# Performance work log

Hardware: AMD Instinct MI355X
Metric: run time of the kernel (lower is better)

Reference implementation:

```python
import jax, jax.numpy as jnp
import numpy as np

H = 768; R = 16; L = 3; NS = 128; NQ = 128


def setup_inputs():
    key = jax.random.key(0)
    ks = iter(jax.random.split(key, 40))
    def w(shape, s=0.02):
        return (s * jax.random.normal(next(ks), shape)).astype(jnp.float32)
    return {
        "support_features": jax.random.normal(next(ks), (NS, H), jnp.float32),
        "support_labels": jax.random.randint(next(ks), (NS,), 0, 3),
        "query_features": jax.random.normal(next(ks), (NQ, H), jnp.float32),
        "sim_w1": w((H, 2 * H)), "sim_b1": jnp.zeros((H,), jnp.float32),
        "sim_w2": w((R, H)), "sim_b2": jnp.zeros((R,), jnp.float32),
        "div_w1": w((H, 2 * H)), "div_b1": jnp.zeros((H,), jnp.float32),
        "div_w2": w((R, H)), "div_b2": jnp.zeros((R,), jnp.float32),
        "rel_w": w((L, R, H, H)), "rel_b": jnp.zeros((L, R, H), jnp.float32),
        "agg_w1": w((L, H, 2 * H)), "agg_b1": jnp.zeros((L, H), jnp.float32),
        "agg_w2": w((L, H, H)), "agg_b2": jnp.zeros((L, H), jnp.float32),
        "ln_g": jnp.ones((L, H), jnp.float32), "ln_b": jnp.zeros((L, H), jnp.float32),
        "cls_w1": w((H // 2, H)), "cls_b1": jnp.zeros((H // 2,), jnp.float32),
        "cls_w2": w((3, H // 2)), "cls_b2": jnp.zeros((3,), jnp.float32),
    }


def _symmetrize(F):
    # torch loop fills [i,j] and [j,i] with value computed from pair (min(i,j), max(i,j)); diag stays 0
    N = F.shape[0]
    idx = jnp.arange(N)
    lower = (idx[:, None] > idx[None, :])
    Fs = jnp.where(lower[:, :, None], jnp.swapaxes(F, 0, 1), F)
    off = (idx[:, None] != idx[None, :]).astype(F.dtype)
    return Fs * off[:, :, None]


def _relations(x, w1, b1, w2, b2, diversity):
    h = x.shape[1]
    wa, wb = w1[:, :h], w1[:, h:]  # split concat([a,b]) @ w1^T into two matmuls
    pa = x @ wa.T                  # [N,H], contribution of first element (x_i)
    if diversity:
        d = jnp.abs(x[:, None, :] - x[None, :, :])   # [N,N,H]
        hid = jax.nn.relu(pa[:, None, :] + d @ wb.T + b1)
    else:
        pb = x @ wb.T
        hid = jax.nn.relu(pa[:, None, :] + pb[None, :, :] + b1)
    logits = hid @ w2.T + b2       # [N,N,R]
    return _symmetrize(jax.nn.softmax(logits, axis=-1))


def _layer_norm(y, g, b):
    mu = y.mean(-1, keepdims=True)
    var = ((y - mu) ** 2).mean(-1, keepdims=True)
    return (y - mu) / jnp.sqrt(var + 1e-5) * g + b


def _prop_layer(x, C, rw, rb, aw1, ab1, aw2, ab2, g, b):
    N = x.shape[0]
    T = jnp.einsum('jh,rkh->jrk', x, rw) + rb       # per-relation transform [N,R,H]
    msg = jnp.einsum('ijr,jrk->ik', C, T) / (N - 1)  # mean over N-1 neighbors (diag of C is 0)
    comb = jnp.concatenate([x, msg], axis=-1)
    agg = jax.nn.relu(comb @ aw1.T + ab1) @ aw2.T + ab2
    return _layer_norm(agg + x, g, b)


def reference(support_features, support_labels, query_features,
              sim_w1, sim_b1, sim_w2, sim_b2,
              div_w1, div_b1, div_w2, div_b2,
              rel_w, rel_b, agg_w1, agg_b1, agg_w2, agg_b2, ln_g, ln_b,
              cls_w1, cls_b1, cls_w2, cls_b2):
    all_x = jnp.concatenate([support_features, query_features], axis=0)
    sim = _relations(all_x, sim_w1, sim_b1, sim_w2, sim_b2, diversity=False)
    div = _relations(all_x, div_w1, div_b1, div_w2, div_b2, diversity=True)
    C = (sim + div) * 0.5
    x = all_x
    for l in range(L):
        x = _prop_layer(x, C, rel_w[l], rel_b[l], agg_w1[l], agg_b1[l],
                        agg_w2[l], agg_b2[l], ln_g[l], ln_b[l])
    q = x[support_features.shape[0]:]
    preds = jax.nn.relu(q @ cls_w1.T + cls_b1) @ cls_w2.T + cls_b2  # dropout = identity (eval)
    return preds, sim, div, x
```

## Files before the change

kernel.cpp:

```cpp
#include <hip/hip_runtime.h>
#include <hip/hip_bf16.h>
#include <hip/hip_fp16.h>


typedef __attribute__((ext_vector_type(8))) short s16x8;
typedef __attribute__((ext_vector_type(4))) float f32x4;

__device__ __forceinline__ short f2bf_s(float f){
  union { __hip_bfloat16 h; short s; } u; u.h = __float2bfloat16(f); return u.s;
}
__device__ __forceinline__ float bf_s2f(short s){
  union { __hip_bfloat16 h; short s; } u; u.s = s; return __bfloat162float(u.h);
}
__device__ __forceinline__ short f2h_s(float f){
  union { __half h; short s; } u; u.h = __float2half(f); return u.s;
}
__device__ __forceinline__ f32x4 mfma16(s16x8 a, s16x8 b, f32x4 c){
  return __builtin_amdgcn_mfma_f32_16x16x32_bf16(a, b, c, 0, 0, 0);
}
__device__ __forceinline__ f32x4 mfma16h(s16x8 a, s16x8 b, f32x4 c){
  return __builtin_amdgcn_mfma_f32_16x16x32_f16(a, b, c, 0, 0, 0);
}
__device__ __forceinline__ void gload16(void* lds, const void* g){
  __builtin_amdgcn_global_load_lds((const __attribute__((address_space(1))) void*)g,
                                   (__attribute__((address_space(3))) void*)lds,
                                   16, 0, 0);
}
__device__ __forceinline__ unsigned pack2bf(float lo, float hi){
  return __builtin_amdgcn_perm(__float_as_uint(hi), __float_as_uint(lo), 0x07060302u);
}
__device__ __forceinline__ s16x8 absdiff_h(uint4 a, uint4 b){
  union { s16x8 v; unsigned u[4]; } o;
  const unsigned au[4] = {a.x,a.y,a.z,a.w}, bu[4] = {b.x,b.y,b.z,b.w};
  #pragma unroll
  for (int w = 0; w < 4; ++w){
    unsigned d;
    asm("v_pk_add_f16 %0, %1, %2 neg_lo:[0,1] neg_hi:[0,1]"
        : "=v"(d) : "v"(au[w]), "v"(bu[w]));
    o.u[w] = d & 0x7fff7fffu;
  }
  return o.v;
}

__device__ __forceinline__ void tri_decode(int b, int& i0, int& j0){
  int jb = (int)((sqrtf(2.f*(float)b + 1.f) - 1.f)*0.5f);
  while (2*(jb+1)*(jb+2) <= b) ++jb;
  while (2*jb*(jb+1) > b) --jb;
  i0 = (b - 2*jb*(jb+1))*4;
  j0 = jb*16;
}
__device__ __forceinline__ void tri_decode8x32(int b, int& i0, int& j0){
  int jb = (int)((sqrtf(2.f*(float)b + 1.f) - 1.f)*0.5f);
  while (2*(jb+1)*(jb+2) <= b) ++jb;
  while (2*jb*(jb+1) > b) --jb;
  i0 = (b - 2*jb*(jb+1))*8;
  j0 = jb*32;
}

template<int BM, int BN, int EPI>
__global__ __launch_bounds__(256) void gemm_bt2(
    const short* __restrict__ A, int lda,
    const short* __restrict__ B, int ldb,
    float* __restrict__ Cf, short* __restrict__ Cb, int ldc,
    const float* __restrict__ bias, int K, int NT)
{
  __shared__ short As[BM*128];
  __shared__ short Bs[BN*128];
  const int tid = threadIdx.x, lane = tid & 63, wid = tid >> 6;
  const int nt = blockIdx.x % NT, mt = blockIdx.x / NT;
  const int m0 = mt*BM, n0 = nt*BN;
  const int wm0 = (wid>>1)*(BM/2), wn0 = (wid&1)*(BN/2);
  f32x4 acc[BM/32][BN/32] = {};
  for (int k0 = 0; k0 < K; k0 += 128){
    if (k0) __syncthreads();
    #pragma unroll
    for (int q = 0; q < BM/16; ++q){
      const int d = (wid*(BM/16)+q)*1024 + lane*16;
      const int row = d>>8, c = d&255;
      gload16((char*)As + (wid*(BM/16)+q)*1024,
              (const char*)A + (size_t)(m0+row)*lda*2 + (size_t)k0*2 + (c ^ ((row&7)<<4)));
    }
    #pragma unroll
    for (int q = 0; q < BN/16; ++q){
      const int d = (wid*(BN/16)+q)*1024 + lane*16;
      const int row = d>>8, c = d&255;
      gload16((char*)Bs + (wid*(BN/16)+q)*1024,
              (const char*)B + (size_t)(n0+row)*ldb*2 + (size_t)k0*2 + (c ^ ((row&7)<<4)));
    }
    __syncthreads();
    #pragma unroll
    for (int kk = 0; kk < 4; ++kk){
      const int colb = (kk*32 + (lane>>4)*8)*2;
      s16x8 af[BM/32], bfv[BN/32];
      #pragma unroll
      for (int mi = 0; mi < BM/32; ++mi){
        const int row = wm0 + mi*16 + (lane&15);
        af[mi] = *(const s16x8*)((char*)As + row*256 + (colb ^ ((row&7)<<4)));
      }
      #pragma unroll
      for (int ni = 0; ni < BN/32; ++ni){
        const int row = wn0 + ni*16 + (lane&15);
        bfv[ni] = *(const s16x8*)((char*)Bs + row*256 + (colb ^ ((row&7)<<4)));
      }
      #pragma unroll
      for (int mi = 0; mi < BM/32; ++mi)
        #pragma unroll
        for (int ni = 0; ni < BN/32; ++ni)
          acc[mi][ni] = mfma16(af[mi], bfv[ni], acc[mi][ni]);
    }
  }
  #pragma unroll
  for (int mi = 0; mi < BM/32; ++mi){
    #pragma unroll
    for (int ni = 0; ni < BN/32; ++ni){
      const int gcol = n0 + wn0 + ni*16 + (lane&15);
      const float bv = bias[gcol];
      #pragma unroll
      for (int r = 0; r < 4; ++r){
        const int grow = m0 + wm0 + mi*16 + (lane>>4)*4 + r;
        float v = acc[mi][ni][r] + bv;
        if (EPI == 2) v = fmaxf(v, 0.f);
        if (EPI == 3) Cf[(size_t)grow*ldc + gcol] = v;
        else          Cb[(size_t)grow*ldc + gcol] = f2bf_s(v);
      }
    }
  }
}

__global__ __launch_bounds__(256) void gemm_msg(
    const short* __restrict__ A,
    const short* __restrict__ B,
    float* __restrict__ slabs)
{
  __shared__ short As[64*64];
  __shared__ short Bs[64*64];
  const int tid = threadIdx.x, lane = tid & 63, wid = tid >> 6;
  const int mt = blockIdx.x / 12, nt = blockIdx.x % 12;
  const int m0 = mt*64, n0 = nt*64, kc0 = blockIdx.y*512;
  const int wm0 = (wid>>1)*32, wn0 = (wid&1)*32;
  f32x4 acc[2][2] = {};
  for (int s = 0; s < 8; ++s){
    const int k0 = kc0 + s*64;
    if (s) __syncthreads();
    #pragma unroll
    for (int q = 0; q < 2; ++q){
      const int d = (wid*2+q)*1024 + lane*16;
      const int row = d>>7, c = d&127;
      gload16((char*)As + (wid*2+q)*1024,
              (const char*)A + (size_t)(m0+row)*8192 + (size_t)k0*2 + (c ^ ((row&7)<<4)));
    }
    #pragma unroll
    for (int rd = 0; rd < 2; ++rd){
      int ei = rd*2048 + tid*8, kr = ei>>6, nc = ei&63;
      union { uint4 v; short s4[8]; } u;
      u.v = *(const uint4*)(B + (size_t)(k0+kr)*768 + n0 + nc);
      #pragma unroll
      for (int e = 0; e < 8; ++e)
        *(short*)((char*)Bs + (nc+e)*128 + ((kr*2) ^ (((nc+e)&7)<<4))) = u.s4[e];
    }
    __syncthreads();
    #pragma unroll
    for (int kk = 0; kk < 2; ++kk){
      const int colb = (kk*32 + (lane>>4)*8)*2;
      s16x8 af[2], bfv[2];
      #pragma unroll
      for (int mi = 0; mi < 2; ++mi){
        const int row = wm0 + mi*16 + (lane&15);
        af[mi] = *(const s16x8*)((char*)As + row*128 + (colb ^ ((row&7)<<4)));
      }
      #pragma unroll
      for (int ni = 0; ni < 2; ++ni){
        const int row = wn0 + ni*16 + (lane&15);
        bfv[ni] = *(const s16x8*)((char*)Bs + row*128 + (colb ^ ((row&7)<<4)));
      }
      #pragma unroll
      for (int mi = 0; mi < 2; ++mi)
        #pragma unroll
        for (int ni = 0; ni < 2; ++ni)
          acc[mi][ni] = mfma16(af[mi], bfv[ni], acc[mi][ni]);
    }
  }
  float* out = slabs + (size_t)blockIdx.y*196608;
  #pragma unroll
  for (int mi = 0; mi < 2; ++mi)
    #pragma unroll
    for (int ni = 0; ni < 2; ++ni){
      const int gcol = n0 + wn0 + ni*16 + (lane&15);
      #pragma unroll
      for (int r = 0; r < 4; ++r){
        const int grow = m0 + wm0 + mi*16 + (lane>>4)*4 + r;
        out[(size_t)grow*768 + gcol] = acc[mi][ni][r];
      }
    }
}

__global__ void msgsum(const float* __restrict__ slabs, short* __restrict__ comb){
  const int i = (blockIdx.x*256 + threadIdx.x)*4;
  if (i >= 196608) return;
  float4 s = {0.f,0.f,0.f,0.f};
  #pragma unroll
  for (int c = 0; c < 8; ++c){
    float4 v = *(const float4*)(slabs + (size_t)c*196608 + i);
    s.x += v.x; s.y += v.y; s.z += v.z; s.w += v.w;
  }
  const float sc = 1.f/255.f;
  const int row = i/768, col = i%768;
  union { uint2 u; short s4[4]; } o;
  o.s4[0]=f2bf_s(s.x*sc); o.s4[1]=f2bf_s(s.y*sc);
  o.s4[2]=f2bf_s(s.z*sc); o.s4[3]=f2bf_s(s.w*sc);
  *(uint2*)(comb + (size_t)row*1536 + 768 + col) = o.u;
}

__global__ __launch_bounds__(512, 2) void pairrel7(
    const short* __restrict__ xh,
    const short* __restrict__ wbdh,
    const float* __restrict__ P2,
    const short* __restrict__ w2d_g,
    float* __restrict__ Ldp)
{
  __shared__ short Bs[2*256*64];
  const int tid = threadIdx.x, lane = tid & 63, wv = tid >> 6;
  const int ip = wv >> 2, jj = (wv >> 1) & 1, wc = wv & 1;
  int i0, j0; tri_decode8x32(blockIdx.x, i0, j0);
  const int nt = blockIdx.y, n0 = nt*256;

  const short* xjp = xh + (size_t)(j0 + jj*16 + (lane&15))*768 + (lane>>4)*8;
  const short* xib = xh + (size_t)(i0 + 4*ip)*768 + (lane>>4)*8;

  #pragma unroll
  for (int q = 0; q < 4; ++q){
    const int d = (wv*4+q)*1024 + lane*16;
    const int row = d>>7, c = d&127;
    gload16((char*)Bs + (wv*4+q)*1024,
            (const char*)wbdh + (size_t)(n0+row)*1536 + (c ^ ((row&7)<<4)));
  }

  f32x4 acc[4][8] = {};
  for (int t = 0; t < 12; ++t){
    uint4 uja = *(const uint4*)(xjp + t*64);
    uint4 ujb = *(const uint4*)(xjp + t*64 + 32);
    uint4 uia[4], uib[4];
    #pragma unroll
    for (int mi = 0; mi < 4; ++mi){
      uia[mi] = *(const uint4*)(xib + (size_t)mi*768 + t*64);
      uib[mi] = *(const uint4*)(xib + (size_t)mi*768 + t*64 + 32);
    }
    if (t < 11){
      char* dst = (char*)Bs + ((t+1)&1)*32768;
      const char* src = (const char*)wbdh + (size_t)(t+1)*128;
      #pragma unroll
      for (int q = 0; q < 4; ++q){
        const int d = (wv*4+q)*1024 + lane*16;
        const int row = d>>7, c = d&127;
        gload16(dst + (wv*4+q)*1024, src + (size_t)(n0+row)*1536 + (c ^ ((row&7)<<4)));
      }
    }
    __builtin_amdgcn_sched_barrier(0);
    if (t < 11) asm volatile("s_waitcnt vmcnt(14)" ::: "memory");
    else        asm volatile("s_waitcnt vmcnt(10)" ::: "memory");
    __builtin_amdgcn_s_barrier();
    __builtin_amdgcn_sched_barrier(0);
    const char* bufc = (const char*)Bs + (t&1)*32768;
    #pragma unroll
    for (int kk = 0; kk < 2; ++kk){
      s16x8 af[4];
      #pragma unroll
      for (int mi = 0; mi < 4; ++mi)
        af[mi] = absdiff_h(kk ? ujb : uja, kk ? uib[mi] : uia[mi]);
      const int colb = (kk*32 + (lane>>4)*8)*2;
      #pragma unroll
      for (int ni = 0; ni < 8; ++ni){
        const int row = wc*128 + ni*16 + (lane&15);
        s16x8 bv = *(const s16x8*)(bufc + row*128 + (colb ^ ((row&7)<<4)));
        #pragma unroll
        for (int mi = 0; mi < 4; ++mi)
          acc[mi][ni] = mfma16h(af[mi], bv, acc[mi][ni]);
      }
    }
    __builtin_amdgcn_sched_barrier(0);
    __builtin_amdgcn_s_barrier();
  }
  __syncthreads();

  float* red = (float*)((char*)Bs + 32768);
  const int kh = wv >> 2, rq = wv & 3;
  #pragma unroll
  for (int h = 0; h < 4; ++h){
    if (ip == (h>>1)){
      #pragma unroll
      for (int q = 0; q < 2; ++q){
        const int mi = 2*(h&1) + q;
        const float* pr = P2 + (size_t)(i0 + 4*ip + mi)*2304 + 1536 + n0;
        #pragma unroll
        for (int ni = 0; ni < 8; ++ni){
          const int col = wc*128 + ni*16 + (lane&15);
          const float pav = pr[col];
          #pragma unroll
          for (int r = 0; r < 4; ++r){
            const int lrow = q*32 + jj*16 + (lane>>4)*4 + r;
            const float v = fmaxf(acc[mi][ni][r] + pav, 0.f);
            *(short*)((char*)Bs + lrow*512 + ((col*2) ^ ((lrow&7)<<4))) =
                (short)(__float_as_uint(v) >> 16);
          }
        }
      }
    }
    __syncthreads();
    f32x4 a2 = {0.f,0.f,0.f,0.f};
    const int arow = rq*16 + (lane&15);
    #pragma unroll
    for (int qq = 0; qq < 4; ++qq){
      const int k = kh*128 + qq*32 + (lane>>4)*8;
      s16x8 a = *(const s16x8*)((char*)Bs + arow*512 + ((k*2) ^ ((arow&7)<<4)));
      s16x8 w = *(const s16x8*)(w2d_g + (size_t)(lane&15)*768 + n0 + k);
      a2 = mfma16(a, w, a2);
    }
    if (kh == 1){
      #pragma unroll
      for (int r = 0; r < 4; ++r)
        red[(rq*16 + (lane>>4)*4 + r)*16 + (lane&15)] = a2[r];
    }
    __syncthreads();
    if (kh == 0){
      #pragma unroll
      for (int r = 0; r < 4; ++r){
        const int lrow = rq*16 + (lane>>4)*4 + r;
        const int p = h*64 + lrow;
        const int i = i0 + (p>>5), j = j0 + (p&31);
        Ldp[(size_t)nt*1048576 + (((size_t)i<<8) + j)*16 + (lane&15)]
          = a2[r] + red[lrow*16 + (lane&15)];
      }
    }
    __syncthreads();
  }
}

__global__ __launch_bounds__(256) void simfused(
    const float* __restrict__ P2,
    const short* __restrict__ w2s_g,
    const float* __restrict__ Ldp,
    const float* __restrict__ b2s, const float* __restrict__ b2d,
    float* __restrict__ simo, float* __restrict__ divo, short* __restrict__ CBo)
{
  __shared__ short Hs[64*256];
  const int tid = threadIdx.x, lane = tid & 63, wv = tid >> 6;
  int i0, j0; tri_decode(blockIdx.x, i0, j0);
  const int arow = wv*16 + (lane&15);
  f32x4 acc2 = {0.f,0.f,0.f,0.f};
  for (int nt = 0; nt < 3; ++nt){
    const int n0 = nt*256;
    if (nt) __syncthreads();
    {
      const int row = tid>>2, c0 = (tid&3)*64;
      const float* pap = P2 + (size_t)(i0 + (row>>4))*2304 + n0 + c0;
      const float* pbp = P2 + (size_t)(j0 + (row&15))*2304 + 768 + n0 + c0;
      #pragma unroll
      for (int cc = 0; cc < 64; cc += 8){
        float4 a0 = *(const float4*)(pap+cc), a1 = *(const float4*)(pap+cc+4);
        float4 q0 = *(const float4*)(pbp+cc), q1 = *(const float4*)(pbp+cc+4);
        uint4 o;
        o.x = pack2bf(fmaxf(a0.x+q0.x,0.f), fmaxf(a0.y+q0.y,0.f));
        o.y = pack2bf(fmaxf(a0.z+q0.z,0.f), fmaxf(a0.w+q0.w,0.f));
        o.z = pack2bf(fmaxf(a1.x+q1.x,0.f), fmaxf(a1.y+q1.y,0.f));
        o.w = pack2bf(fmaxf(a1.z+q1.z,0.f), fmaxf(a1.w+q1.w,0.f));
        *(uint4*)((char*)Hs + row*512 + (((c0+cc)*2) ^ ((row&7)<<4))) = o;
      }
    }
    __syncthreads();
    #pragma unroll
    for (int q = 0; q < 8; ++q){
      const int colb = (q*32 + (lane>>4)*8)*2;
      s16x8 a = *(const s16x8*)((const char*)Hs + arow*512 + (colb ^ ((arow&7)<<4)));
      s16x8 w = *(const s16x8*)(w2s_g + (size_t)(lane&15)*768 + n0 + q*32 + (lane>>4)*8);
      acc2 = mfma16(a, w, acc2);
    }
  }
  const int r_ = lane & 15;
  const float bs_ = b2s[r_], bd_ = b2d[r_];
  #pragma unroll
  for (int r = 0; r < 4; ++r){
    const int p = wv*16 + (lane>>4)*4 + r;
    const int i = i0 + (p>>4), j = j0 + (p&15);
    if (j < i) continue;
    if (j == i){
      const size_t pii = (((size_t)i<<8) + i)*16 + r_;
      simo[pii] = 0.f; divo[pii] = 0.f; CBo[pii] = 0;
      continue;
    }
    const size_t base = (((size_t)i<<8) + j)*16;
    const float sv = acc2[r] + bs_;
    const float dv = Ldp[base+r_] + Ldp[base+1048576+r_] + Ldp[base+2097152+r_] + bd_;
    float m = sv;
    m = fmaxf(m, __shfl_xor(m,1)); m = fmaxf(m, __shfl_xor(m,2));
    m = fmaxf(m, __shfl_xor(m,4)); m = fmaxf(m, __shfl_xor(m,8));
    float e = expf(sv - m), s = e;
    s += __shfl_xor(s,1); s += __shfl_xor(s,2); s += __shfl_xor(s,4); s += __shfl_xor(s,8);
    const float so = e/s;
    m = dv;
    m = fmaxf(m, __shfl_xor(m,1)); m = fmaxf(m, __shfl_xor(m,2));
    m = fmaxf(m, __shfl_xor(m,4)); m = fmaxf(m, __shfl_xor(m,8));
    e = expf(dv - m); s = e;
    s += __shfl_xor(s,1); s += __shfl_xor(s,2); s += __shfl_xor(s,4); s += __shfl_xor(s,8);
    const float dd = e/s;
    const size_t pij = base + r_;
    const size_t pji = (((size_t)j<<8) + i)*16 + r_;
    simo[pij] = so; simo[pji] = so;
    divo[pij] = dd; divo[pji] = dd;
    const short cb = f2bf_s(0.5f*(so + dd));
    CBo[pij] = cb; CBo[pji] = cb;
  }
}

__global__ __launch_bounds__(512) void gemm_relT(
    const short* __restrict__ A,
    const float* __restrict__ Bf,
    short* __restrict__ T,
    const float* __restrict__ bias)
{
  __shared__ short As[256*64];
  __shared__ short Bs[64*64];
  const int tid = threadIdx.x, lane = tid & 63, wv = tid >> 6;
  const int n0 = blockIdx.x*64;
  const int wm = wv >> 1, wn = wv & 1;
  const int brow = tid >> 3, c0 = (tid & 7)*8;
  f32x4 acc[4][2] = {};
  for (int k0 = 0; k0 < 768; k0 += 64){
    if (k0) __syncthreads();
    #pragma unroll
    for (int q = 0; q < 4; ++q){
      const int d = (wv*4+q)*1024 + lane*16;
      const int row = d>>7, c = d&127;
      gload16((char*)As + (wv*4+q)*1024,
              (const char*)A + (size_t)row*3072 + (size_t)k0*2 + (c ^ ((row&7)<<4)));
    }
    {
      const float* bp = Bf + (size_t)(n0+brow)*768 + k0 + c0;
      float4 v0 = *(const float4*)bp, v1 = *(const float4*)(bp+4);
      union { uint4 v; unsigned u[4]; } uo;
      uo.u[0]=pack2bf(v0.x,v0.y); uo.u[1]=pack2bf(v0.z,v0.w);
      uo.u[2]=pack2bf(v1.x,v1.y); uo.u[3]=pack2bf(v1.z,v1.w);
      *(uint4*)((char*)Bs + brow*128 + (((c0*2)) ^ ((brow&7)<<4))) = uo.v;
    }
    __syncthreads();
    #pragma unroll
    for (int kk = 0; kk < 2; ++kk){
      const int kb = kk*64 + (lane>>4)*16;
      s16x8 af[4], bfv[2];
      #pragma unroll
      for (int mi = 0; mi < 4; ++mi){
        const int row = wm*64 + mi*16 + (lane&15);
        af[mi] = *(const s16x8*)((char*)As + row*128 + (kb ^ ((row&7)<<4)));
      }
      #pragma unroll
      for (int ni = 0; ni < 2; ++ni){
        const int row = wn*32 + ni*16 + (lane&15);
        bfv[ni] = *(const s16x8*)((char*)Bs + row*128 + (kb ^ ((row&7)<<4)));
      }
      #pragma unroll
      for (int mi = 0; mi < 4; ++mi)
        #pragma unroll
        for (int ni = 0; ni < 2; ++ni)
          acc[mi][ni] = mfma16(af[mi], bfv[ni], acc[mi][ni]);
    }
  }
  #pragma unroll
  for (int mi = 0; mi < 4; ++mi)
    #pragma unroll
    for (int ni = 0; ni < 2; ++ni){
      const int nn = n0 + wn*32 + ni*16 + (lane&15);
      const float bv = bias[nn];
      #pragma unroll
      for (int r = 0; r < 4; ++r){
        const int row = wm*64 + mi*16 + (lane>>4)*4 + r;
        T[(size_t)row*12288 + nn] = f2bf_s(acc[mi][ni][r] + bv);
      }
    }
}

__global__ __launch_bounds__(256) void ln_kernel(
    const float* __restrict__ y, float* __restrict__ x, short* __restrict__ combx,
    const float* __restrict__ g, const float* __restrict__ b, float* __restrict__ xfinal)
{
  const int row = blockIdx.x, tid = threadIdx.x;
  float tv[3]; float s = 0.f, s2 = 0.f;
  #pragma unroll
  for (int c = 0; c < 3; ++c){
    const int idx = tid + c*256;
    const float v = y[row*768+idx] + x[row*768+idx];
    tv[c] = v; s += v; s2 += v*v;
  }
  #pragma unroll
  for (int off = 32; off > 0; off >>= 1){ s += __shfl_down(s, off); s2 += __shfl_down(s2, off); }
  __shared__ float red[8];
  const int wid = tid >> 6, lane = tid & 63;
  if (lane == 0){ red[wid] = s; red[wid+4] = s2; }
  __syncthreads();
  if (tid == 0){
    red[0] = red[0]+red[1]+red[2]+red[3];
    red[4] = red[4]+red[5]+red[6]+red[7];
  }
  __syncthreads();
  const float mu = red[0]*(1.f/768.f);
  const float var = red[4]*(1.f/768.f) - mu*mu;
  const float inv = rsqrtf(var + 1e-5f);
  #pragma unroll
  for (int c = 0; c < 3; ++c){
    const int idx = tid + c*256;
    const float v = (tv[c]-mu)*inv*g[idx] + b[idx];
    x[row*768+idx] = v;
    combx[(size_t)row*1536 + idx] = f2bf_s(v);
    if (xfinal) xfinal[row*768+idx] = v;
  }
}

__device__ __forceinline__ void cvt4(const float* __restrict__ s,
                                     short* __restrict__ d, int i, int n){
  if (i >= n) return;
  float4 v = *(const float4*)(s+i);
  union { uint2 u; short s4[4]; } o;
  o.s4[0]=f2bf_s(v.x); o.s4[1]=f2bf_s(v.y); o.s4[2]=f2bf_s(v.z); o.s4[3]=f2bf_s(v.w);
  *(uint2*)(d+i) = o.u;
}

__global__ void setup_all(
    const float* __restrict__ sim_w2, const float* __restrict__ div_w2,
    const float* __restrict__ agg_w1, const float* __restrict__ agg_w2,
    const float* __restrict__ cls_w1, const float* __restrict__ sim_w1,
    const float* __restrict__ div_w1, const float* __restrict__ sup,
    const float* __restrict__ qry, const float* __restrict__ sim_b1,
    const float* __restrict__ div_b1,
    short* __restrict__ W2S, short* __restrict__ W2D, short* __restrict__ AW1,
    short* __restrict__ AW2, short* __restrict__ CW1, short* __restrict__ W1X4,
    float* __restrict__ XF, short* __restrict__ COMB, float* __restrict__ B1C,
    short* __restrict__ XH, short* __restrict__ WBDH)
{
  const int b = blockIdx.x, tid = threadIdx.x;
  if (b < 12)        cvt4(sim_w2, W2S, (b*256+tid)*4, 12288);
  else if (b < 24)   cvt4(div_w2, W2D, ((b-12)*256+tid)*4, 12288);
  else if (b < 3480) cvt4(agg_w1, AW1, ((b-24)*256+tid)*4, 3538944);
  else if (b < 5208) cvt4(agg_w2, AW2, ((b-3480)*256+tid)*4, 1769472);
  else if (b < 5496) cvt4(cls_w1, CW1, ((b-5208)*256+tid)*4, 294912);
  else if (b < 7800){
    const int i = ((b-5496)*256+tid)*4;
    if (i < 2359296){
      const int mat = i / 589824, rem = i % 589824;
      const int r = rem / 768, c = rem % 768;
      const float* src = (mat < 2 ? sim_w1 : div_w1) + (size_t)r*1536 + (mat&1)*768 + c;
      float4 v = *(const float4*)src;
      union { uint2 u; short s4[4]; } o;
      o.s4[0]=f2bf_s(v.x); o.s4[1]=f2bf_s(v.y); o.s4[2]=f2bf_s(v.z); o.s4[3]=f2bf_s(v.w);
      *(uint2*)(W1X4+i) = o.u;
    }
  } else if (b < 7992){
    const int i = ((b-7800)*256+tid)*4;
    if (i < 196608){
      const int row = i / 768, col = i % 768;
      const float* s = (row < 128 ? sup + (size_t)row*768 : qry + (size_t)(row-128)*768) + col;
      float4 v = *(const float4*)s;
      *(float4*)(XF+i) = v;
      union { uint2 u; short s4[4]; } o;
      o.s4[0]=f2bf_s(v.x); o.s4[1]=f2bf_s(v.y); o.s4[2]=f2bf_s(v.z); o.s4[3]=f2bf_s(v.w);
      *(uint2*)(COMB + (size_t)row*1536 + col) = o.u;
      union { uint2 u; short s4[4]; } oh;
      oh.s4[0]=f2h_s(v.x); oh.s4[1]=f2h_s(v.y); oh.s4[2]=f2h_s(v.z); oh.s4[3]=f2h_s(v.w);
      *(uint2*)(XH + i) = oh.u;
    }
  } else if (b < 7993){
    for (int t = tid; t < 2304; t += 256)
      B1C[t] = (t < 768) ? sim_b1[t] : ((t < 1536) ? 0.f : div_b1[t-1536]);
  } else {
    const int i = ((b-7993)*256+tid)*4;
    if (i < 589824){
      const int r = i / 768, c = i % 768;
      float4 v = *(const float4*)(div_w1 + (size_t)r*1536 + 768 + c);
      union { uint2 u; short s4[4]; } o;
      o.s4[0]=f2h_s(v.x); o.s4[1]=f2h_s(v.y); o.s4[2]=f2h_s(v.z); o.s4[3]=f2h_s(v.w);
      *(uint2*)(WBDH + i) = o.u;
    }
  }
}

__global__ void cls2_kernel(const short* __restrict__ hc, const float* __restrict__ w2,
                            const float* __restrict__ b2, float* __restrict__ preds){
  const int t = blockIdx.x*192 + threadIdx.x;
  if (t >= 384) return;
  const int m = t/3, c = t - m*3;
  float s = b2[c];
  for (int k = 0; k < 384; ++k)
    s += bf_s2f(hc[m*384+k]) * w2[c*384+k];
  preds[m*3+c] = s;
}

static const size_t OFF_B1CAT = 0;
static const size_t OFF_MSGF  = 4210688;
static const size_t OFF_LDP   = 10502144;
static const size_t OFF_P     = 23085056;
static const size_t OFF_XF    = 25444352;
static const size_t OFF_Y     = 26230784;
static const size_t OFF_COMB  = 27017216;
static const size_t OFF_CB    = 27803648;
static const size_t OFF_W1X4  = 29900800;
static const size_t OFF_W2S   = 34619392;
static const size_t OFF_W2D   = 34643968;
static const size_t OFF_AW1   = 34668544;
static const size_t OFF_AW2   = 41746432;
static const size_t OFF_CW1   = 45285376;
static const size_t OFF_TBUF  = 45875200;
static const size_t OFF_HID1  = 52166656;
static const size_t OFF_HIDC  = 52559872;
static const size_t OFF_XH    = 52658176;
static const size_t OFF_WBDH  = 53051392;

extern "C" void kernel_launch(void* const* d_in, const int* in_sizes, int n_in,
                              void* d_out, int out_size, void* d_ws, size_t ws_size,
                              hipStream_t stream)
{
  (void)in_sizes; (void)n_in; (void)out_size; (void)ws_size;
  const float* sup    = (const float*)d_in[0];
  const float* qry    = (const float*)d_in[2];
  const float* sim_w1 = (const float*)d_in[3];
  const float* sim_b1 = (const float*)d_in[4];
  const float* sim_w2 = (const float*)d_in[5];
  const float* sim_b2 = (const float*)d_in[6];
  const float* div_w1 = (const float*)d_in[7];
  const float* div_b1 = (const float*)d_in[8];
  const float* div_w2 = (const float*)d_in[9];
  const float* div_b2 = (const float*)d_in[10];
  const float* rel_w  = (const float*)d_in[11];
  const float* rel_b  = (const float*)d_in[12];
  const float* agg_w1 = (const float*)d_in[13];
  const float* agg_b1 = (const float*)d_in[14];
  const float* agg_w2 = (const float*)d_in[15];
  const float* agg_b2 = (const float*)d_in[16];
  const float* ln_g   = (const float*)d_in[17];
  const float* ln_b   = (const float*)d_in[18];
  const float* cls_w1 = (const float*)d_in[19];
  const float* cls_b1 = (const float*)d_in[20];
  const float* cls_w2 = (const float*)d_in[21];
  const float* cls_b2 = (const float*)d_in[22];

  char* w = (char*)d_ws;
  float* B1C  = (float*)(w + OFF_B1CAT);
  float* MSGF = (float*)(w + OFF_MSGF);
  float* LDP  = (float*)(w + OFF_LDP);
  float* P2   = (float*)(w + OFF_P);
  float* XF   = (float*)(w + OFF_XF);
  float* Y    = (float*)(w + OFF_Y);
  short* COMB = (short*)(w + OFF_COMB);
  short* CB   = (short*)(w + OFF_CB);
  short* W1X4 = (short*)(w + OFF_W1X4);
  short* W2S  = (short*)(w + OFF_W2S);
  short* W2D  = (short*)(w + OFF_W2D);
  short* AW1  = (short*)(w + OFF_AW1);
  short* AW2  = (short*)(w + OFF_AW2);
  short* CW1  = (short*)(w + OFF_CW1);
  short* TBUF = (short*)(w + OFF_TBUF);
  short* HID1 = (short*)(w + OFF_HID1);
  short* HIDC = (short*)(w + OFF_HIDC);
  short* XH   = (short*)(w + OFF_XH);
  short* WBDH = (short*)(w + OFF_WBDH);

  float* preds = (float*)d_out;
  float* simo  = preds + 384;
  float* divo  = simo + 1048576;
  float* xout  = divo + 1048576;

  setup_all<<<8569, 256, 0, stream>>>(sim_w2, div_w2, agg_w1, agg_w2, cls_w1,
                                      sim_w1, div_w1, sup, qry, sim_b1, div_b1,
                                      W2S, W2D, AW1, AW2, CW1, W1X4, XF, COMB, B1C,
                                      XH, WBDH);

  gemm_bt2<32,64,3><<<288, 256, 0, stream>>>(COMB, 1536, W1X4, 768, P2, nullptr, 2304,
                                             B1C, 768, 36);

  pairrel7<<<dim3(144,3), 512, 0, stream>>>(XH, WBDH, P2, W2D, LDP);
  simfused<<<544, 256, 0, stream>>>(P2, W2S, LDP, sim_b2, div_b2, simo, divo, CB);

  for (int l = 0; l < 3; ++l){
    gemm_relT<<<192, 512, 0, stream>>>(COMB, rel_w + (size_t)l*9437184, TBUF,
                                       rel_b + l*12288);
    gemm_msg<<<dim3(48,8), 256, 0, stream>>>(CB, TBUF, MSGF);
    msgsum<<<192, 256, 0, stream>>>(MSGF, COMB);
    gemm_bt2<32,32,2><<<192, 256, 0, stream>>>(COMB, 1536, AW1 + (size_t)l*1179648, 1536,
                                               nullptr, HID1, 768, agg_b1 + l*768, 1536, 24);
    gemm_bt2<32,32,3><<<192, 256, 0, stream>>>(HID1, 768, AW2 + (size_t)l*589824, 768,
                                               Y, nullptr, 768, agg_b2 + l*768, 768, 24);
    ln_kernel<<<256, 256, 0, stream>>>(Y, XF, COMB, ln_g + l*768, ln_b + l*768,
                                       (l == 2) ? xout : nullptr);
  }

  gemm_bt2<32,32,2><<<48, 256, 0, stream>>>(COMB + (size_t)128*1536, 1536, CW1, 768,
                                            nullptr, HIDC, 384, cls_b1, 768, 12);
  cls2_kernel<<<2, 192, 0, stream>>>(HIDC, cls_w2, cls_b2, preds);
}
```

Baseline: 309.7 us.

## Fuse propagation layers and classifier into one cooperative persistent kernel

```diff
diff --git a/kernel.cpp b/kernel.cpp
--- a/kernel.cpp
+++ b/kernel.cpp
@@ -1,6 +1,9 @@
 #include <hip/hip_runtime.h>
 #include <hip/hip_bf16.h>
 #include <hip/hip_fp16.h>
+#include <hip/hip_cooperative_groups.h>
+
+namespace cg = cooperative_groups;
 
 
 typedef __attribute__((ext_vector_type(8))) short s16x8;
@@ -127,16 +130,153 @@
   }
 }
 
-__global__ __launch_bounds__(256) void gemm_msg(
-    const short* __restrict__ A,
-    const short* __restrict__ B,
-    float* __restrict__ slabs)
-{
-  __shared__ short As[64*64];
-  __shared__ short Bs[64*64];
+template<int BM, int BN, int EPI>
+__device__ __forceinline__ void gemm_dev(char* smem_, int b,
+    const short* A, int lda, const short* B, int ldb,
+    float* Cf, short* Cb, int ldc, const float* bias, int K, int NT)
+{
+  short* As = (short*)smem_;
+  short* Bs = (short*)(smem_ + (size_t)BM*256);
   const int tid = threadIdx.x, lane = tid & 63, wid = tid >> 6;
-  const int mt = blockIdx.x / 12, nt = blockIdx.x % 12;
-  const int m0 = mt*64, n0 = nt*64, kc0 = blockIdx.y*512;
+  const int nt = b % NT, mt = b / NT;
+  const int m0 = mt*BM, n0 = nt*BN;
+  const int wm0 = (wid>>1)*(BM/2), wn0 = (wid&1)*(BN/2);
+  f32x4 acc[BM/32][BN/32] = {};
+  for (int k0 = 0; k0 < K; k0 += 128){
+    if (k0) __syncthreads();
+    #pragma unroll
+    for (int q = 0; q < BM/16; ++q){
+      const int d = (wid*(BM/16)+q)*1024 + lane*16;
+      const int row = d>>8, c = d&255;
+      gload16((char*)As + (wid*(BM/16)+q)*1024,
+              (const char*)A + (size_t)(m0+row)*lda*2 + (size_t)k0*2 + (c ^ ((row&7)<<4)));
+    }
+    #pragma unroll
+    for (int q = 0; q < BN/16; ++q){
+      const int d = (wid*(BN/16)+q)*1024 + lane*16;
+      const int row = d>>8, c = d&255;
+      gload16((char*)Bs + (wid*(BN/16)+q)*1024,
+              (const char*)B + (size_t)(n0+row)*ldb*2 + (size_t)k0*2 + (c ^ ((row&7)<<4)));
+    }
+    __syncthreads();
+    #pragma unroll
+    for (int kk = 0; kk < 4; ++kk){
+      const int colb = (kk*32 + (lane>>4)*8)*2;
+      s16x8 af[BM/32], bfv[BN/32];
+      #pragma unroll
+      for (int mi = 0; mi < BM/32; ++mi){
+        const int row = wm0 + mi*16 + (lane&15);
+        af[mi] = *(const s16x8*)((char*)As + row*256 + (colb ^ ((row&7)<<4)));
+      }
+      #pragma unroll
+      for (int ni = 0; ni < BN/32; ++ni){
+        const int row = wn0 + ni*16 + (lane&15);
+        bfv[ni] = *(const s16x8*)((char*)Bs + row*256 + (colb ^ ((row&7)<<4)));
+      }
+      #pragma unroll
+      for (int mi = 0; mi < BM/32; ++mi)
+        #pragma unroll
+        for (int ni = 0; ni < BN/32; ++ni)
+          acc[mi][ni] = mfma16(af[mi], bfv[ni], acc[mi][ni]);
+    }
+  }
+  __syncthreads();
+  #pragma unroll
+  for (int mi = 0; mi < BM/32; ++mi){
+    #pragma unroll
+    for (int ni = 0; ni < BN/32; ++ni){
+      const int gcol = n0 + wn0 + ni*16 + (lane&15);
+      const float bv = bias[gcol];
+      #pragma unroll
+      for (int r = 0; r < 4; ++r){
+        const int grow = m0 + wm0 + mi*16 + (lane>>4)*4 + r;
+        float v = acc[mi][ni][r] + bv;
+        if (EPI == 2) v = fmaxf(v, 0.f);
+        if (EPI == 3) Cf[(size_t)grow*ldc + gcol] = v;
+        else          Cb[(size_t)grow*ldc + gcol] = f2bf_s(v);
+      }
+    }
+  }
+}
+
+__device__ __forceinline__ void relT_dev(char* smem_, int b,
+    const short* A, const float* Bf, short* T, const float* bias)
+{
+  short* As = (short*)smem_;
+  short* Bs = (short*)(smem_ + 16384);
+  const int tid = threadIdx.x, lane = tid & 63, wv = tid >> 6;
+  const int nt = b >> 1, mt = b & 1;
+  const int n0 = nt*64, m0 = mt*128;
+  const int wm = wv >> 1, wn = wv & 1;
+  const int brow = tid >> 2, q4 = tid & 3;
+  f32x4 acc[4][2] = {};
+  for (int k0 = 0; k0 < 768; k0 += 64){
+    if (k0) __syncthreads();
+    #pragma unroll
+    for (int q = 0; q < 4; ++q){
+      const int d = (wv*4+q)*1024 + lane*16;
+      const int row = d>>7, c = d&127;
+      gload16((char*)As + (wv*4+q)*1024,
+              (const char*)A + (size_t)(m0+row)*3072 + (size_t)k0*2 + (c ^ ((row&7)<<4)));
+    }
+    {
+      const float* bp = Bf + (size_t)(n0+brow)*768 + k0 + q4*16;
+      float4 v0 = *(const float4*)bp,      v1 = *(const float4*)(bp+4);
+      float4 v2 = *(const float4*)(bp+8),  v3 = *(const float4*)(bp+12);
+      union { uint4 v; unsigned u[4]; } ua, ub;
+      ua.u[0]=pack2bf(v0.x,v0.y); ua.u[1]=pack2bf(v0.z,v0.w);
+      ua.u[2]=pack2bf(v1.x,v1.y); ua.u[3]=pack2bf(v1.z,v1.w);
+      ub.u[0]=pack2bf(v2.x,v2.y); ub.u[1]=pack2bf(v2.z,v2.w);
+      ub.u[2]=pack2bf(v3.x,v3.y); ub.u[3]=pack2bf(v3.z,v3.w);
+      const int bc = q4*32;
+      *(uint4*)((char*)Bs + brow*128 + ((bc   ) ^ ((brow&7)<<4))) = ua.v;
+      *(uint4*)((char*)Bs + brow*128 + ((bc+16) ^ ((brow&7)<<4))) = ub.v;
+    }
+    __syncthreads();
+    #pragma unroll
+    for (int kk = 0; kk < 2; ++kk){
+      const int kb = kk*64 + (lane>>4)*16;
+      s16x8 af[4], bfv[2];
+      #pragma unroll
+      for (int mi = 0; mi < 4; ++mi){
+        const int row = wm*64 + mi*16 + (lane&15);
+        af[mi] = *(const s16x8*)((char*)As + row*128 + (kb ^ ((row&7)<<4)));
+      }
+      #pragma unroll
+      for (int ni = 0; ni < 2; ++ni){
+        const int row = wn*32 + ni*16 + (lane&15);
+        bfv[ni] = *(const s16x8*)((char*)Bs + row*128 + (kb ^ ((row&7)<<4)));
+      }
+      #pragma unroll
+      for (int mi = 0; mi < 4; ++mi)
+        #pragma unroll
+        for (int ni = 0; ni < 2; ++ni)
+          acc[mi][ni] = mfma16(af[mi], bfv[ni], acc[mi][ni]);
+    }
+  }
+  __syncthreads();
+  #pragma unroll
+  for (int mi = 0; mi < 4; ++mi)
+    #pragma unroll
+    for (int ni = 0; ni < 2; ++ni){
+      const int nn = n0 + wn*32 + ni*16 + (lane&15);
+      const float bv = bias[nn];
+      #pragma unroll
+      for (int r = 0; r < 4; ++r){
+        const int row = m0 + wm*64 + mi*16 + (lane>>4)*4 + r;
+        T[(size_t)row*12288 + nn] = f2bf_s(acc[mi][ni][r] + bv);
+      }
+    }
+}
+
+__device__ __forceinline__ void msg_dev(char* smem_, int t48, int kc,
+    const short* A, const short* B, float* slabs)
+{
+  short* As = (short*)smem_;
+  short* Bs = (short*)(smem_ + 8192);
+  const int tid = threadIdx.x, lane = tid & 63, wid = tid >> 6;
+  const int mt = t48 / 12, nt = t48 % 12;
+  const int m0 = mt*64, n0 = nt*64, kc0 = kc*512;
   const int wm0 = (wid>>1)*32, wn0 = (wid&1)*32;
   f32x4 acc[2][2] = {};
   for (int s = 0; s < 8; ++s){
@@ -180,7 +320,8 @@
           acc[mi][ni] = mfma16(af[mi], bfv[ni], acc[mi][ni]);
     }
   }
-  float* out = slabs + (size_t)blockIdx.y*196608;
+  __syncthreads();
+  float* out = slabs + (size_t)kc*196608;
   #pragma unroll
   for (int mi = 0; mi < 2; ++mi)
     #pragma unroll
@@ -194,21 +335,103 @@
     }
 }
 
-__global__ void msgsum(const float* __restrict__ slabs, short* __restrict__ comb){
-  const int i = (blockIdx.x*256 + threadIdx.x)*4;
-  if (i >= 196608) return;
-  float4 s = {0.f,0.f,0.f,0.f};
-  #pragma unroll
-  for (int c = 0; c < 8; ++c){
-    float4 v = *(const float4*)(slabs + (size_t)c*196608 + i);
-    s.x += v.x; s.y += v.y; s.z += v.z; s.w += v.w;
-  }
-  const float sc = 1.f/255.f;
-  const int row = i/768, col = i%768;
-  union { uint2 u; short s4[4]; } o;
-  o.s4[0]=f2bf_s(s.x*sc); o.s4[1]=f2bf_s(s.y*sc);
-  o.s4[2]=f2bf_s(s.z*sc); o.s4[3]=f2bf_s(s.w*sc);
-  *(uint2*)(comb + (size_t)row*1536 + 768 + col) = o.u;
+__device__ __forceinline__ void ln_dev(char* smem_, int row,
+    const float* y, float* x, short* combx,
+    const float* g, const float* b, float* xfinal)
+{
+  float* red = (float*)smem_;
+  const int tid = threadIdx.x;
+  float tv[3]; float s = 0.f, s2 = 0.f;
+  #pragma unroll
+  for (int c = 0; c < 3; ++c){
+    const int idx = tid + c*256;
+    const float v = y[row*768+idx] + x[row*768+idx];
+    tv[c] = v; s += v; s2 += v*v;
+  }
+  #pragma unroll
+  for (int off = 32; off > 0; off >>= 1){ s += __shfl_down(s, off); s2 += __shfl_down(s2, off); }
+  const int wid = tid >> 6, lane = tid & 63;
+  if (lane == 0){ red[wid] = s; red[wid+4] = s2; }
+  __syncthreads();
+  if (tid == 0){
+    red[0] = red[0]+red[1]+red[2]+red[3];
+    red[4] = red[4]+red[5]+red[6]+red[7];
+  }
+  __syncthreads();
+  const float mu = red[0]*(1.f/768.f);
+  const float var = red[4]*(1.f/768.f) - mu*mu;
+  const float inv = rsqrtf(var + 1e-5f);
+  #pragma unroll
+  for (int c = 0; c < 3; ++c){
+    const int idx = tid + c*256;
+    const float v = (tv[c]-mu)*inv*g[idx] + b[idx];
+    x[row*768+idx] = v;
+    combx[(size_t)row*1536 + idx] = f2bf_s(v);
+    if (xfinal) xfinal[row*768+idx] = v;
+  }
+}
+
+__global__ __launch_bounds__(256) void layers_coop(
+    const float* rel_w, const float* rel_b,
+    short* COMB, const short* CB, short* TBUF, float* MSGF,
+    const short* AW1, const float* agg_b1,
+    const short* AW2, const float* agg_b2,
+    const float* ln_g, const float* ln_b,
+    float* XF, float* Y, short* HID1, float* xout,
+    const short* CW1, const float* cls_b1, short* HIDC,
+    const float* cls_w2, const float* cls_b2, float* preds)
+{
+  cg::grid_group grid = cg::this_grid();
+  __shared__ char smem[24576];
+  const int gb = blockIdx.x, tid = threadIdx.x;
+
+  for (int l = 0; l < 3; ++l){
+    for (int b = gb; b < 384; b += 256)
+      relT_dev(smem, b, COMB, rel_w + (size_t)l*9437184, TBUF, rel_b + l*12288);
+    grid.sync();
+    for (int b = gb; b < 384; b += 256)
+      msg_dev(smem, b % 48, b / 48, CB, TBUF, MSGF);
+    grid.sync();
+    if (gb < 192){
+      const int i = (gb*256 + tid)*4;
+      float4 s = {0.f,0.f,0.f,0.f};
+      #pragma unroll
+      for (int c = 0; c < 8; ++c){
+        float4 v = *(const float4*)(MSGF + (size_t)c*196608 + i);
+        s.x += v.x; s.y += v.y; s.z += v.z; s.w += v.w;
+      }
+      const float sc = 1.f/255.f;
+      const int row = i/768, col = i%768;
+      union { uint2 u; short s4[4]; } o;
+      o.s4[0]=f2bf_s(s.x*sc); o.s4[1]=f2bf_s(s.y*sc);
+      o.s4[2]=f2bf_s(s.z*sc); o.s4[3]=f2bf_s(s.w*sc);
+      *(uint2*)(COMB + (size_t)row*1536 + 768 + col) = o.u;
+    }
+    grid.sync();
+    if (gb < 192)
+      gemm_dev<32,32,2>(smem, gb, COMB, 1536, AW1 + (size_t)l*1179648, 1536,
+                        nullptr, HID1, 768, agg_b1 + l*768, 1536, 24);
+    grid.sync();
+    if (gb < 192)
+      gemm_dev<32,32,3>(smem, gb, HID1, 768, AW2 + (size_t)l*589824, 768,
+                        Y, nullptr, 768, agg_b2 + l*768, 768, 24);
+    grid.sync();
+    ln_dev(smem, gb, Y, XF, COMB, ln_g + l*768, ln_b + l*768,
+           (l == 2) ? xout : nullptr);
+    grid.sync();
+  }
+  if (gb < 48)
+    gemm_dev<32,32,2>(smem, gb, COMB + (size_t)128*1536, 1536, CW1, 768,
+                      nullptr, HIDC, 384, cls_b1, 768, 12);
+  grid.sync();
+  if (gb < 2 && tid < 192){
+    const int t = gb*192 + tid;
+    const int m = t/3, c = t - m*3;
+    float s = cls_b2[c];
+    for (int k = 0; k < 384; ++k)
+      s += bf_s2f(HIDC[m*384+k]) * cls_w2[c*384+k];
+    preds[m*3+c] = s;
+  }
 }
 
 __global__ __launch_bounds__(512, 2) void pairrel7(
@@ -411,108 +634,6 @@
   }
 }
 
-__global__ __launch_bounds__(512) void gemm_relT(
-    const short* __restrict__ A,
-    const float* __restrict__ Bf,
-    short* __restrict__ T,
-    const float* __restrict__ bias)
-{
-  __shared__ short As[256*64];
-  __shared__ short Bs[64*64];
-  const int tid = threadIdx.x, lane = tid & 63, wv = tid >> 6;
-  const int n0 = blockIdx.x*64;
-  const int wm = wv >> 1, wn = wv & 1;
-  const int brow = tid >> 3, c0 = (tid & 7)*8;
-  f32x4 acc[4][2] = {};
-  for (int k0 = 0; k0 < 768; k0 += 64){
-    if (k0) __syncthreads();
-    #pragma unroll
-    for (int q = 0; q < 4; ++q){
-      const int d = (wv*4+q)*1024 + lane*16;
-      const int row = d>>7, c = d&127;
-      gload16((char*)As + (wv*4+q)*1024,
-              (const char*)A + (size_t)row*3072 + (size_t)k0*2 + (c ^ ((row&7)<<4)));
-    }
-    {
-      const float* bp = Bf + (size_t)(n0+brow)*768 + k0 + c0;
-      float4 v0 = *(const float4*)bp, v1 = *(const float4*)(bp+4);
-      union { uint4 v; unsigned u[4]; } uo;
-      uo.u[0]=pack2bf(v0.x,v0.y); uo.u[1]=pack2bf(v0.z,v0.w);
-      uo.u[2]=pack2bf(v1.x,v1.y); uo.u[3]=pack2bf(v1.z,v1.w);
-      *(uint4*)((char*)Bs + brow*128 + (((c0*2)) ^ ((brow&7)<<4))) = uo.v;
-    }
-    __syncthreads();
-    #pragma unroll
-    for (int kk = 0; kk < 2; ++kk){
-      const int kb = kk*64 + (lane>>4)*16;
-      s16x8 af[4], bfv[2];
-      #pragma unroll
-      for (int mi = 0; mi < 4; ++mi){
-        const int row = wm*64 + mi*16 + (lane&15);
-        af[mi] = *(const s16x8*)((char*)As + row*128 + (kb ^ ((row&7)<<4)));
-      }
-      #pragma unroll
-      for (int ni = 0; ni < 2; ++ni){
-        const int row = wn*32 + ni*16 + (lane&15);
-        bfv[ni] = *(const s16x8*)((char*)Bs + row*128 + (kb ^ ((row&7)<<4)));
-      }
-      #pragma unroll
-      for (int mi = 0; mi < 4; ++mi)
-        #pragma unroll
-        for (int ni = 0; ni < 2; ++ni)
-          acc[mi][ni] = mfma16(af[mi], bfv[ni], acc[mi][ni]);
-    }
-  }
-  #pragma unroll
-  for (int mi = 0; mi < 4; ++mi)
-    #pragma unroll
-    for (int ni = 0; ni < 2; ++ni){
-      const int nn = n0 + wn*32 + ni*16 + (lane&15);
-      const float bv = bias[nn];
-      #pragma unroll
-      for (int r = 0; r < 4; ++r){
-        const int row = wm*64 + mi*16 + (lane>>4)*4 + r;
-        T[(size_t)row*12288 + nn] = f2bf_s(acc[mi][ni][r] + bv);
-      }
-    }
-}
-
-__global__ __launch_bounds__(256) void ln_kernel(
-    const float* __restrict__ y, float* __restrict__ x, short* __restrict__ combx,
-    const float* __restrict__ g, const float* __restrict__ b, float* __restrict__ xfinal)
-{
-  const int row = blockIdx.x, tid = threadIdx.x;
-  float tv[3]; float s = 0.f, s2 = 0.f;
-  #pragma unroll
-  for (int c = 0; c < 3; ++c){
-    const int idx = tid + c*256;
-    const float v = y[row*768+idx] + x[row*768+idx];
-    tv[c] = v; s += v; s2 += v*v;
-  }
-  #pragma unroll
-  for (int off = 32; off > 0; off >>= 1){ s += __shfl_down(s, off); s2 += __shfl_down(s2, off); }
-  __shared__ float red[8];
-  const int wid = tid >> 6, lane = tid & 63;
-  if (lane == 0){ red[wid] = s; red[wid+4] = s2; }
-  __syncthreads();
-  if (tid == 0){
-    red[0] = red[0]+red[1]+red[2]+red[3];
-    red[4] = red[4]+red[5]+red[6]+red[7];
-  }
-  __syncthreads();
-  const float mu = red[0]*(1.f/768.f);
-  const float var = red[4]*(1.f/768.f) - mu*mu;
-  const float inv = rsqrtf(var + 1e-5f);
-  #pragma unroll
-  for (int c = 0; c < 3; ++c){
-    const int idx = tid + c*256;
-    const float v = (tv[c]-mu)*inv*g[idx] + b[idx];
-    x[row*768+idx] = v;
-    combx[(size_t)row*1536 + idx] = f2bf_s(v);
-    if (xfinal) xfinal[row*768+idx] = v;
-  }
-}
-
 __device__ __forceinline__ void cvt4(const float* __restrict__ s,
                                      short* __restrict__ d, int i, int n){
   if (i >= n) return;
@@ -578,17 +699,6 @@
       *(uint2*)(WBDH + i) = o.u;
     }
   }
-}
-
-__global__ void cls2_kernel(const short* __restrict__ hc, const float* __restrict__ w2,
-                            const float* __restrict__ b2, float* __restrict__ preds){
-  const int t = blockIdx.x*192 + threadIdx.x;
-  if (t >= 384) return;
-  const int m = t/3, c = t - m*3;
-  float s = b2[c];
-  for (int k = 0; k < 384; ++k)
-    s += bf_s2f(hc[m*384+k]) * w2[c*384+k];
-  preds[m*3+c] = s;
 }
 
 static const size_t OFF_B1CAT = 0;
@@ -676,20 +786,13 @@
   pairrel7<<<dim3(144,3), 512, 0, stream>>>(XH, WBDH, P2, W2D, LDP);
   simfused<<<544, 256, 0, stream>>>(P2, W2S, LDP, sim_b2, div_b2, simo, divo, CB);
 
-  for (int l = 0; l < 3; ++l){
-    gemm_relT<<<192, 512, 0, stream>>>(COMB, rel_w + (size_t)l*9437184, TBUF,
-                                       rel_b + l*12288);
-    gemm_msg<<<dim3(48,8), 256, 0, stream>>>(CB, TBUF, MSGF);
-    msgsum<<<192, 256, 0, stream>>>(MSGF, COMB);
-    gemm_bt2<32,32,2><<<192, 256, 0, stream>>>(COMB, 1536, AW1 + (size_t)l*1179648, 1536,
-                                               nullptr, HID1, 768, agg_b1 + l*768, 1536, 24);
-    gemm_bt2<32,32,3><<<192, 256, 0, stream>>>(HID1, 768, AW2 + (size_t)l*589824, 768,
-                                               Y, nullptr, 768, agg_b2 + l*768, 768, 24);
-    ln_kernel<<<256, 256, 0, stream>>>(Y, XF, COMB, ln_g + l*768, ln_b + l*768,
-                                       (l == 2) ? xout : nullptr);
-  }
-
-  gemm_bt2<32,32,2><<<48, 256, 0, stream>>>(COMB + (size_t)128*1536, 1536, CW1, 768,
-                                            nullptr, HIDC, 384, cls_b1, 768, 12);
-  cls2_kernel<<<2, 192, 0, stream>>>(HIDC, cls_w2, cls_b2, preds);
-}
+  void* cargs[] = {
+    (void*)&rel_w, (void*)&rel_b, (void*)&COMB, (void*)&CB, (void*)&TBUF,
+    (void*)&MSGF, (void*)&AW1, (void*)&agg_b1, (void*)&AW2, (void*)&agg_b2,
+    (void*)&ln_g, (void*)&ln_b, (void*)&XF, (void*)&Y, (void*)&HID1,
+    (void*)&xout, (void*)&CW1, (void*)&cls_b1, (void*)&HIDC, (void*)&cls_w2,
+    (void*)&cls_b2, (void*)&preds
+  };
+  hipLaunchCooperativeKernel((const void*)layers_coop, dim3(256), dim3(256),
+                             cargs, 0, stream);
+}
```

After: 911.8 us. +194.4%, slower.
